# Performance work log

Measured on AMD Instinct MI355X. Metric: run time of the kernel, lower is better.

## Reference

```python
import jax, jax.numpy as jnp
import numpy as np

N_NODES = 40000
N_EDGES = 640000
D_IN = 128
D_OUT = 128


def setup_inputs() -> dict:
    key = jax.random.key(0)
    k1, k2, k3, k4, k5 = jax.random.split(key, 5)
    feature = jax.random.normal(k1, (N_NODES, D_IN), dtype=jnp.float32)
    src_idx = jax.random.randint(k2, (N_EDGES,), 0, N_NODES, dtype=jnp.int64)
    dst_idx = jax.random.randint(k3, (N_EDGES,), 0, N_NODES, dtype=jnp.int64)
    W = jax.random.normal(k4, (D_OUT, D_IN), dtype=jnp.float32) * (1.0 / np.sqrt(D_IN))
    b = jax.random.normal(k5, (D_OUT,), dtype=jnp.float32) * 0.01
    return {"feature": feature, "src_idx": src_idx, "dst_idx": dst_idx, "W": W, "b": b}


def reference(feature, src_idx, dst_idx, W, b):
    # u_mul_v: per-edge message = x[src] * x[dst]   [E, D]
    msg = feature[src_idx] * feature[dst_idx]
    # mean aggregation at destination nodes (nodes with no in-edges get 0, like DGL)
    summed = jax.ops.segment_sum(msg, dst_idx, num_segments=N_NODES)  # [N, D]
    cnt = jax.ops.segment_sum(jnp.ones((msg.shape[0],), dtype=feature.dtype),
                              dst_idx, num_segments=N_NODES)  # [N]
    x = summed / jnp.maximum(cnt, 1.0)[:, None]
    # final linear: x @ W.T + b
    return x @ W.T + b
```

## Files before the change

### kernel.cpp

```cpp
#include <hip/hip_runtime.h>

#define N_NODES 40000
#define N_EDGES 640000
#define D 128
#define CAP 64
#define PREP_GRID 1280
#define XPITCH 136

typedef __attribute__((ext_vector_type(8))) short short8;
typedef __attribute__((ext_vector_type(4))) float float4v;

static __device__ __forceinline__ unsigned bf16_rne(float f) {
    unsigned u = __float_as_uint(f);
    return (u + 0x7FFFu + ((u >> 16) & 1u)) >> 16;
}
static __device__ __forceinline__ unsigned pack2(float a, float b) {
    return bf16_rne(a) | (bf16_rne(b) << 16);
}

__global__ __launch_bounds__(256) void prep_kernel(
    const float* __restrict__ feat,
    const int*   __restrict__ src,
    const int*   __restrict__ dst,
    const float* __restrict__ W,
    unsigned*       __restrict__ featb,
    unsigned*       __restrict__ wfrag,
    int*            __restrict__ deg,
    unsigned short* __restrict__ bucket)
{
    const int g  = blockIdx.x * 256 + threadIdx.x;
    const int GT = PREP_GRID * 256;

    {
        const int e0 = g;
        const int e1 = g + GT;
        const bool h1 = e1 < N_EDGES;
        int d0 = dst[e0];
        int s0 = src[e0];
        int d1 = h1 ? dst[e1] : 0;
        int s1 = h1 ? src[e1] : 0;
        int r0 = atomicAdd(&deg[d0], 1);
        int r1 = h1 ? atomicAdd(&deg[d1], 1) : CAP;
        if (r0 < CAP) bucket[(size_t)d0 * CAP + r0] = (unsigned short)s0;
        if (r1 < CAP) bucket[(size_t)d1 * CAP + r1] = (unsigned short)s1;
    }

    for (int i = g; i < N_NODES * D / 4; i += GT) {
        float4 f = reinterpret_cast<const float4*>(feat)[i];
        uint2 p;
        p.x = pack2(f.x, f.y);
        p.y = pack2(f.z, f.w);
        reinterpret_cast<uint2*>(featb)[i] = p;
    }

    if (g < 32 * 64) {
        const int tile = g >> 6, lane = g & 63;
        const int nt = tile >> 2, kt = tile & 3;
        const int n = nt * 16 + (lane & 15);
        const int k = kt * 32 + (lane >> 4) * 8;
        const float* wp = W + (size_t)n * D + k;
        uint4 p;
        p.x = pack2(wp[0], wp[1]);
        p.y = pack2(wp[2], wp[3]);
        p.z = pack2(wp[4], wp[5]);
        p.w = pack2(wp[6], wp[7]);
        reinterpret_cast<uint4*>(wfrag)[g] = p;
    }
}

__global__ __launch_bounds__(512) void agg_gemm(
    const float*          __restrict__ feat,
    const unsigned*       __restrict__ featb,
    const unsigned*       __restrict__ wfrag,
    const int*            __restrict__ deg,
    const unsigned short* __restrict__ bucket,
    const float*          __restrict__ bias,
    float*                __restrict__ out)
{
    __shared__ float xs[16 * XPITCH];
    const int t     = threadIdx.x;
    const int wave  = t >> 6;
    const int lane  = t & 63;
    const int node0 = blockIdx.x * 16;

    const int n0  = node0 + wave * 2;
    const int dg0 = min(deg[n0],     CAP);
    const int dg1 = min(deg[n0 + 1], CAP);
    const unsigned iw0 = reinterpret_cast<const unsigned*>(bucket + (size_t)n0 * CAP)[lane & 31];
    const unsigned iw1 = reinterpret_cast<const unsigned*>(bucket + (size_t)(n0 + 1) * CAP)[lane & 31];

    float2 acc0 = make_float2(0.f, 0.f);
    float2 acc1 = make_float2(0.f, 0.f);

    #define IDX0(i) ({ int w_ = __shfl((int)iw0, (i) >> 1, 64); ((i) & 1) ? ((w_ >> 16) & 0xFFFF) : (w_ & 0xFFFF); })
    #define IDX1(i) ({ int w_ = __shfl((int)iw1, (i) >> 1, 64); ((i) & 1) ? ((w_ >> 16) & 0xFFFF) : (w_ & 0xFFFF); })

    int i0 = 0, i1 = 0;
    while (i0 + 8 <= dg0 && i1 + 8 <= dg1) {
        unsigned va[8], vb[8];
        #pragma unroll
        for (int j = 0; j < 8; ++j) va[j] = featb[((size_t)IDX0(i0 + j) << 6) + lane];
        #pragma unroll
        for (int j = 0; j < 8; ++j) vb[j] = featb[((size_t)IDX1(i1 + j) << 6) + lane];
        #pragma unroll
        for (int j = 0; j < 8; ++j) {
            acc0.x += __uint_as_float(va[j] << 16);
            acc0.y += __uint_as_float(va[j] & 0xFFFF0000u);
            acc1.x += __uint_as_float(vb[j] << 16);
            acc1.y += __uint_as_float(vb[j] & 0xFFFF0000u);
        }
        i0 += 8; i1 += 8;
    }
    for (; i0 + 8 <= dg0; i0 += 8) {
        unsigned va[8];
        #pragma unroll
        for (int j = 0; j < 8; ++j) va[j] = featb[((size_t)IDX0(i0 + j) << 6) + lane];
        #pragma unroll
        for (int j = 0; j < 8; ++j) {
            acc0.x += __uint_as_float(va[j] << 16);
            acc0.y += __uint_as_float(va[j] & 0xFFFF0000u);
        }
    }
    for (; i0 < dg0; ++i0) {
        unsigned v = featb[((size_t)IDX0(i0) << 6) + lane];
        acc0.x += __uint_as_float(v << 16);
        acc0.y += __uint_as_float(v & 0xFFFF0000u);
    }
    for (; i1 + 8 <= dg1; i1 += 8) {
        unsigned vb[8];
        #pragma unroll
        for (int j = 0; j < 8; ++j) vb[j] = featb[((size_t)IDX1(i1 + j) << 6) + lane];
        #pragma unroll
        for (int j = 0; j < 8; ++j) {
            acc1.x += __uint_as_float(vb[j] << 16);
            acc1.y += __uint_as_float(vb[j] & 0xFFFF0000u);
        }
    }
    for (; i1 < dg1; ++i1) {
        unsigned v = featb[((size_t)IDX1(i1) << 6) + lane];
        acc1.x += __uint_as_float(v << 16);
        acc1.y += __uint_as_float(v & 0xFFFF0000u);
    }
    #undef IDX0
    #undef IDX1

    {
        const float2 fd0 = reinterpret_cast<const float2*>(feat + (size_t)n0 * D)[lane];
        const float2 fd1 = reinterpret_cast<const float2*>(feat + (size_t)(n0 + 1) * D)[lane];
        const float inv0 = 1.0f / (float)max(dg0, 1);
        const float inv1 = 1.0f / (float)max(dg1, 1);
        xs[(wave * 2)     * XPITCH + lane * 2]     = acc0.x * fd0.x * inv0;
        xs[(wave * 2)     * XPITCH + lane * 2 + 1] = acc0.y * fd0.y * inv0;
        xs[(wave * 2 + 1) * XPITCH + lane * 2]     = acc1.x * fd1.x * inv1;
        xs[(wave * 2 + 1) * XPITCH + lane * 2 + 1] = acc1.y * fd1.y * inv1;
    }
    __syncthreads();

    {
        const int arow = lane & 15;
        const int aq   = lane >> 4;
        const int col  = lane & 15;

        short8 afrag[4];
        #pragma unroll
        for (int kt = 0; kt < 4; ++kt) {
            const float* xp = xs + arow * XPITCH + kt * 32 + aq * 8;
            union { short8 s; unsigned u[4]; } af;
            af.u[0] = pack2(xp[0], xp[1]);
            af.u[1] = pack2(xp[2], xp[3]);
            af.u[2] = pack2(xp[4], xp[5]);
            af.u[3] = pack2(xp[6], xp[7]);
            afrag[kt] = af.s;
        }

        float bo = bias[wave * 16 + col];
        float4v acc = (float4v){bo, bo, bo, bo};

        #pragma unroll
        for (int kt = 0; kt < 4; ++kt) {
            union { short8 s; uint4 u; } bf;
            bf.u = reinterpret_cast<const uint4*>(wfrag)[(wave * 4 + kt) * 64 + lane];
            acc = __builtin_amdgcn_mfma_f32_16x16x32_bf16(afrag[kt], bf.s, acc, 0, 0, 0);
        }

        const int rbase = (lane >> 4) * 4;
        const int c = wave * 16 + col;
        #pragma unroll
        for (int r = 0; r < 4; ++r)
            out[(size_t)(node0 + rbase + r) * D + c] = acc[r];
    }
}

extern "C" void kernel_launch(void* const* d_in, const int* in_sizes, int n_in,
                              void* d_out, int out_size, void* d_ws, size_t ws_size,
                              hipStream_t stream)
{
    const float* feat = (const float*)d_in[0];
    const int*   src  = (const int*)  d_in[1];
    const int*   dst  = (const int*)  d_in[2];
    const float* W    = (const float*)d_in[3];
    const float* bias = (const float*)d_in[4];
    float* out = (float*)d_out;

    unsigned*       featb  = (unsigned*)d_ws;
    unsigned*       wfrag  = featb + (size_t)N_NODES * D / 2;
    unsigned short* bucket = (unsigned short*)(wfrag + 8192);
    int*            deg    = (int*)(bucket + (size_t)N_NODES * CAP);

    hipMemsetAsync(deg, 0, N_NODES * sizeof(int), stream);
    prep_kernel<<<PREP_GRID, 256, 0, stream>>>(feat, src, dst, W, featb, wfrag, deg, bucket);
    agg_gemm<<<N_NODES / 16, 512, 0, stream>>>(feat, featb, wfrag, deg, bucket, bias, out);
}
```

Measured before the change: 139.9 us.

## Split per-node edge buckets into eight slabs to spread atomic contention

The single degree counter and 64-slot bucket per node become eight slabs of counters and 16-slot buckets, with the slab chosen by block index. The goal is to cut atomic contention and cross-XCD traffic during bucket building. The aggregation kernel compacts up to 8 entries per slab into a shared-memory index list for the main gather loop, then handles any overflow entries (slots 8 to 15) in a slow scalar loop. The cost is a memset eight times larger, extra prefix and shuffle work, and a shared-memory compaction step that relies on only a block-level fence rather than a barrier.

```diff
diff --git a/kernel.cpp b/kernel.cpp
--- a/kernel.cpp
+++ b/kernel.cpp
@@ -3,7 +3,9 @@
 #define N_NODES 40000
 #define N_EDGES 640000
 #define D 128
-#define CAP 64
+#define NSLAB 8
+#define CAPV 16
+#define CAPF 8
 #define PREP_GRID 1280
 #define XPITCH 136
 
@@ -25,11 +27,14 @@
     const float* __restrict__ W,
     unsigned*       __restrict__ featb,
     unsigned*       __restrict__ wfrag,
-    int*            __restrict__ deg,
-    unsigned short* __restrict__ bucket)
+    int*            __restrict__ vdeg,
+    unsigned short* __restrict__ vb16)
 {
     const int g  = blockIdx.x * 256 + threadIdx.x;
     const int GT = PREP_GRID * 256;
+    const int v8 = blockIdx.x & 7;
+    int*            dmy = vdeg + (size_t)v8 * N_NODES;
+    unsigned short* bmy = vb16 + (size_t)v8 * N_NODES * CAPV;
 
     {
         const int e0 = g;
@@ -39,10 +44,10 @@
         int s0 = src[e0];
         int d1 = h1 ? dst[e1] : 0;
         int s1 = h1 ? src[e1] : 0;
-        int r0 = atomicAdd(&deg[d0], 1);
-        int r1 = h1 ? atomicAdd(&deg[d1], 1) : CAP;
-        if (r0 < CAP) bucket[(size_t)d0 * CAP + r0] = (unsigned short)s0;
-        if (r1 < CAP) bucket[(size_t)d1 * CAP + r1] = (unsigned short)s1;
+        int r0 = atomicAdd(&dmy[d0], 1);
+        int r1 = h1 ? atomicAdd(&dmy[d1], 1) : CAPV;
+        if (r0 < CAPV) bmy[(size_t)d0 * CAPV + r0] = (unsigned short)s0;
+        if (r1 < CAPV) bmy[(size_t)d1 * CAPV + r1] = (unsigned short)s1;
     }
 
     for (int i = g; i < N_NODES * D / 4; i += GT) {
@@ -72,22 +77,53 @@
     const float*          __restrict__ feat,
     const unsigned*       __restrict__ featb,
     const unsigned*       __restrict__ wfrag,
-    const int*            __restrict__ deg,
-    const unsigned short* __restrict__ bucket,
+    const int*            __restrict__ vdeg,
+    const unsigned short* __restrict__ vb16,
     const float*          __restrict__ bias,
     float*                __restrict__ out)
 {
     __shared__ float xs[16 * XPITCH];
+    __shared__ unsigned idxw[8][2][32];
     const int t     = threadIdx.x;
     const int wave  = t >> 6;
     const int lane  = t & 63;
     const int node0 = blockIdx.x * 16;
 
-    const int n0  = node0 + wave * 2;
-    const int dg0 = min(deg[n0],     CAP);
-    const int dg1 = min(deg[n0 + 1], CAP);
-    const unsigned iw0 = reinterpret_cast<const unsigned*>(bucket + (size_t)n0 * CAP)[lane & 31];
-    const unsigned iw1 = reinterpret_cast<const unsigned*>(bucket + (size_t)(n0 + 1) * CAP)[lane & 31];
+    const int n0 = node0 + wave * 2;
+    const int n1 = n0 + 1;
+
+    int cl = 0;
+    if (lane < 16) cl = vdeg[(size_t)(lane & 7) * N_NODES + ((lane < 8) ? n0 : n1)];
+
+    int dgt0 = 0, dgt1 = 0;
+    int c0f[8], c1f[8];
+    int pf0 = 0, pf1 = 0;
+    #pragma unroll
+    for (int u = 0; u < 8; ++u) {
+        int cu0 = __shfl(cl, u, 64);
+        int cu1 = __shfl(cl, u + 8, 64);
+        dgt0 += cu0; dgt1 += cu1;
+        c0f[u] = min(cu0, CAPF); c1f[u] = min(cu1, CAPF);
+        pf0 += c0f[u]; pf1 += c1f[u];
+    }
+
+    {
+        const int v = lane >> 3, s = lane & 7;
+        unsigned short q0 = vb16[((size_t)v * N_NODES + n0) * CAPV + s];
+        unsigned short q1 = vb16[((size_t)v * N_NODES + n1) * CAPV + s];
+        int pfx0 = 0, pfx1 = 0;
+        #pragma unroll
+        for (int u = 0; u < 8; ++u) {
+            if (u < v) { pfx0 += c0f[u]; pfx1 += c1f[u]; }
+        }
+        if (s < c0f[v]) ((unsigned short*)idxw[wave][0])[pfx0 + s] = q0;
+        if (s < c1f[v]) ((unsigned short*)idxw[wave][1])[pfx1 + s] = q1;
+    }
+    __threadfence_block();
+
+    const unsigned iw0 = idxw[wave][0][lane & 31];
+    const unsigned iw1 = idxw[wave][1][lane & 31];
+    const int dg0 = pf0, dg1 = pf1;
 
     float2 acc0 = make_float2(0.f, 0.f);
     float2 acc1 = make_float2(0.f, 0.f);
@@ -144,11 +180,36 @@
     #undef IDX0
     #undef IDX1
 
+    if (dgt0 != pf0) {
+        #pragma unroll 1
+        for (int u = 0; u < 8; ++u) {
+            int cu = min(__shfl(cl, u, 64), CAPV);
+            for (int s = CAPF; s < cu; ++s) {
+                unsigned short idx = vb16[((size_t)u * N_NODES + n0) * CAPV + s];
+                unsigned v = featb[((size_t)idx << 6) + lane];
+                acc0.x += __uint_as_float(v << 16);
+                acc0.y += __uint_as_float(v & 0xFFFF0000u);
+            }
+        }
+    }
+    if (dgt1 != pf1) {
+        #pragma unroll 1
+        for (int u = 0; u < 8; ++u) {
+            int cu = min(__shfl(cl, u + 8, 64), CAPV);
+            for (int s = CAPF; s < cu; ++s) {
+                unsigned short idx = vb16[((size_t)u * N_NODES + n1) * CAPV + s];
+                unsigned v = featb[((size_t)idx << 6) + lane];
+                acc1.x += __uint_as_float(v << 16);
+                acc1.y += __uint_as_float(v & 0xFFFF0000u);
+            }
+        }
+    }
+
     {
         const float2 fd0 = reinterpret_cast<const float2*>(feat + (size_t)n0 * D)[lane];
-        const float2 fd1 = reinterpret_cast<const float2*>(feat + (size_t)(n0 + 1) * D)[lane];
-        const float inv0 = 1.0f / (float)max(dg0, 1);
-        const float inv1 = 1.0f / (float)max(dg1, 1);
+        const float2 fd1 = reinterpret_cast<const float2*>(feat + (size_t)n1 * D)[lane];
+        const float inv0 = 1.0f / (float)max(dgt0, 1);
+        const float inv1 = 1.0f / (float)max(dgt1, 1);
         xs[(wave * 2)     * XPITCH + lane * 2]     = acc0.x * fd0.x * inv0;
         xs[(wave * 2)     * XPITCH + lane * 2 + 1] = acc0.y * fd0.y * inv0;
         xs[(wave * 2 + 1) * XPITCH + lane * 2]     = acc1.x * fd1.x * inv1;
@@ -202,12 +263,12 @@
     const float* bias = (const float*)d_in[4];
     float* out = (float*)d_out;
 
-    unsigned*       featb  = (unsigned*)d_ws;
-    unsigned*       wfrag  = featb + (size_t)N_NODES * D / 2;
-    unsigned short* bucket = (unsigned short*)(wfrag + 8192);
-    int*            deg    = (int*)(bucket + (size_t)N_NODES * CAP);
-
-    hipMemsetAsync(deg, 0, N_NODES * sizeof(int), stream);
-    prep_kernel<<<PREP_GRID, 256, 0, stream>>>(feat, src, dst, W, featb, wfrag, deg, bucket);
-    agg_gemm<<<N_NODES / 16, 512, 0, stream>>>(feat, featb, wfrag, deg, bucket, bias, out);
-}
+    unsigned*       featb = (unsigned*)d_ws;
+    unsigned*       wfrag = featb + (size_t)N_NODES * D / 2;
+    unsigned short* vb16  = (unsigned short*)(wfrag + 8192);
+    int*            vdeg  = (int*)(vb16 + (size_t)NSLAB * N_NODES * CAPV);
+
+    hipMemsetAsync(vdeg, 0, (size_t)NSLAB * N_NODES * sizeof(int), stream);
+    prep_kernel<<<PREP_GRID, 256, 0, stream>>>(feat, src, dst, W, featb, wfrag, vdeg, vb16);
+    agg_gemm<<<N_NODES / 16, 512, 0, stream>>>(feat, featb, wfrag, vdeg, vb16, bias, out);
+}
```

Measured after the change: 145.6 us. 1.04x slower.
